# Kernel tuning notes

Measured on AMD Instinct MI355X. Metric: run time of the kernel, lower is better.

The kernel has to match this reference:

```python
import jax, jax.numpy as jnp
import numpy as np

INPUT_SIZE = 1024
HIDDEN_SIZE = 1024
BATCH = 32768
LEARNING_RATE = 0.01
# First call: time_stamps is empty -> temporal_weight = 1.0
TEMPORAL_WEIGHT = 1.0


def setup_inputs() -> dict:
    key = jax.random.key(0)
    kx, kw = jax.random.split(key)
    x = jax.random.normal(kx, (BATCH, INPUT_SIZE), dtype=jnp.float32)
    # nn.Parameter(torch.randn(input_size, hidden_size) * 0.1)
    W = jax.random.normal(kw, (INPUT_SIZE, HIDDEN_SIZE), dtype=jnp.float32) * 0.1
    return {"x": x, "W": W}


def reference(x, W):
    # Forward: hidden = tanh(x @ W)
    hidden = jnp.tanh(x @ W)  # [B, H]
    # Hebbian update: sum_b lr * outer(x_b, hidden_b) * w(t) / B == lr * w(t)/B * x^T @ hidden
    batch = x.shape[0]
    delta_w = (LEARNING_RATE * TEMPORAL_WEIGHT / batch) * (x.T @ hidden)  # [I, H]
    new_W = jnp.clip(W + delta_w, -1.0, 1.0)
    return hidden, new_W
```

## Files before the change

kernel.cpp:

```cpp
#include <hip/hip_runtime.h>
#include <hip/hip_fp8.h>
#include <cstdint>

#define BB 32768
#define II 1024
#define HH 1024
#define SPLIT 16
#define KCH (BB/SPLIT)
#define NT1 (II/64)
#define NT2 (KCH/64)

typedef _Float16 f16;
typedef _Float16 f16x4 __attribute__((ext_vector_type(4)));
typedef _Float16 f16x8 __attribute__((ext_vector_type(8)));
typedef float f32x4 __attribute__((ext_vector_type(4)));

typedef const __attribute__((address_space(1))) void gvoid_t;
typedef __attribute__((address_space(3))) void lvoid_t;

__device__ __forceinline__ void gload16(const void* g, void* l){
    __builtin_amdgcn_global_load_lds((gvoid_t*)g, (lvoid_t*)l, 16, 0, 0);
}

__device__ __forceinline__ float tanh_fast(float s){
    float a = fabsf(s);
    float e = __expf(-2.0f * a);
    float t = __fdividef(1.0f - e, 1.0f + e);
    return s < 0.0f ? -t : t;
}

__device__ __forceinline__ unsigned char f2fp8(float v){
    __hip_fp8_e4m3 q(v);
    return (unsigned char)q.__x;
}

__global__ __launch_bounds__(256) void k_prep2(const float* __restrict__ x,
                                               f16* __restrict__ xf,
                                               unsigned char* __restrict__ xt8,
                                               const float* __restrict__ W,
                                               f16* __restrict__ wt){
    __shared__ float lt[64*67];
    const int t = threadIdx.x;
    const int bx = (int)blockIdx.x;
    const bool isX = (bx < 512);
    const float* in = isX ? x : W;
    const int C = isX ? II : HH, R = isX ? BB : II;
    const int r0 = (isX ? bx : bx-512)*64;
    const int c0 = blockIdx.y*64;
    #pragma unroll
    for (int p=0; p<4; ++p){
        int r = p*16 + (t>>4);
        int c = (t&15)*4;
        f32x4 v = __builtin_nontemporal_load((const f32x4*)&in[(size_t)(r0+r)*C + c0 + c]);
        if (isX){
            f16x4 hv = {(f16)v[0],(f16)v[1],(f16)v[2],(f16)v[3]};
            *(f16x4*)&xf[(size_t)(r0+r)*C + c0 + c] = hv;
        }
        lt[r*67 + c+0] = v[0];
        lt[r*67 + c+1] = v[1];
        lt[r*67 + c+2] = v[2];
        lt[r*67 + c+3] = v[3];
    }
    __syncthreads();
    const int c = t>>2, rb = (t&3)*16;
    if (isX){
        union { unsigned char cb[16]; f32x4 v4; } u;
        #pragma unroll
        for (int e=0; e<16; ++e) u.cb[e] = f2fp8(lt[(rb+e)*67 + c]);
        *(f32x4*)&xt8[(size_t)(c0+c)*R + r0 + rb] = u.v4;
    } else {
        f16x8 a, b;
        #pragma unroll
        for (int e=0; e<8; ++e) a[e] = (f16)lt[(rb+e)*67 + c];
        #pragma unroll
        for (int e=0; e<8; ++e) b[e] = (f16)lt[(rb+8+e)*67 + c];
        f16* o = &wt[(size_t)(c0+c)*R + r0 + rb];
        *(f16x8*)o = a;
        *(f16x8*)(o+8) = b;
    }
}

__device__ __forceinline__ void stage_half(const f16* __restrict__ panel, int ld,
                                           int row0, int kcol0, char* lds_half,
                                           int wid, int lane){
    #pragma unroll
    for (int r=0;r<2;++r){
        int o = r*8192 + wid*1024 + lane*16;
        int rr = o>>7;
        int c0 = (o&127) ^ ((rr&7)<<4);
        gload16(panel + (size_t)(row0 + rr)*ld + kcol0 + (c0>>1), lds_half + r*8192 + wid*1024);
    }
}

#define RD_A(BUFA, mh) { \
    _Pragma("unroll") for (int m_=0;m_<4;++m_){ \
        af[m_][0] = *(const f16x8*)((BUFA) + rowA + (mh)*8192 + m_*2048 + ksw0); \
        af[m_][1] = *(const f16x8*)((BUFA) + rowA + (mh)*8192 + m_*2048 + ksw1); }}

#define RD_B(BUFB, nh) { \
    _Pragma("unroll") for (int n_=0;n_<2;++n_){ \
        bf[(nh)*2+n_][0] = *(const f16x8*)((BUFB) + rowB + (nh)*4096 + n_*2048 + ksw0); \
        bf[(nh)*2+n_][1] = *(const f16x8*)((BUFB) + rowB + (nh)*4096 + n_*2048 + ksw1); }}

#define MFMA_Q(mh,nh) { \
    __builtin_amdgcn_s_setprio(1); \
    _Pragma("unroll") for (int m_=0;m_<4;++m_){ \
      _Pragma("unroll") for (int n_=0;n_<2;++n_){ \
        _Pragma("unroll") for (int ks_=0;ks_<2;++ks_){ \
          acc[(mh)*4+m_][(nh)*2+n_] = __builtin_amdgcn_mfma_f32_16x16x32_f16( \
              af[m_][ks_], bf[(nh)*2+n_][ks_], acc[(mh)*4+m_][(nh)*2+n_], 0,0,0); }}} \
    __builtin_amdgcn_s_setprio(0); }

#define PH_SYNC1 { __builtin_amdgcn_s_barrier(); \
    asm volatile("s_waitcnt lgkmcnt(0)" ::: "memory"); \
    __builtin_amdgcn_sched_barrier(0); }
#define PH_SYNC2 { __builtin_amdgcn_s_barrier(); }
#define LGKM8 { asm volatile("s_waitcnt lgkmcnt(8)" ::: "memory"); }

__device__ __forceinline__ void kloop8_f16(const f16* __restrict__ Ap, int lda, int arow0,
                                           const f16* __restrict__ Bp, int ldb, int brow0,
                                           int kbase, int nt, char* sm,
                                           f32x4 (&acc)[8][4])
{
    const int t = threadIdx.x, lane = t & 63, wid = t >> 6;
    const int wr = wid >> 2, wc = wid & 3;
    const int fr = lane & 15, kg = lane >> 4;
    const int mask = nt - 1;
    char* const A0 = sm;
    char* const B0 = sm + 32768;
    char* const A1 = sm + 65536;
    char* const B1 = sm + 98304;
    const int rowA = wr*16384 + fr*128;
    const int rowB = (wc>>1)*16384 + (wc&1)*8192 + fr*128;
    const int ksw0 = ((kg    ) ^ (fr & 7)) << 4;
    const int ksw1 = ((kg + 4) ^ (fr & 7)) << 4;

    f16x8 af[4][2], bf[4][2];

    stage_half(Ap, lda, arow0 +   0, kbase +  0, A0,         wid, lane);
    stage_half(Ap, lda, arow0 + 128, kbase +  0, A0 + 16384, wid, lane);
    stage_half(Bp, ldb, brow0 +   0, kbase +  0, B0,         wid, lane);
    stage_half(Bp, ldb, brow0 + 128, kbase +  0, B0 + 16384, wid, lane);
    stage_half(Bp, ldb, brow0 +   0, kbase + 64, B1,         wid, lane);
    stage_half(Ap, lda, arow0 +   0, kbase + 64, A1,         wid, lane);
    asm volatile("s_waitcnt vmcnt(4)" ::: "memory");
    __builtin_amdgcn_s_barrier();

    const int ni = nt >> 1;
    for (int it = 0; it < ni; ++it){
        const int k1 = (2*it + 1) * 64;
        const int k2 = ((2*it + 2) & mask) * 64;
        const int k3 = ((2*it + 3) & mask) * 64;
        RD_A(A0, 0); RD_B(B0, 0);
        stage_half(Ap, lda, arow0 + 128, kbase + k1, A1 + 16384, wid, lane);
        LGKM8; PH_SYNC1; MFMA_Q(0,0); PH_SYNC2;
        RD_B(B0, 1);
        stage_half(Bp, ldb, brow0 + 128, kbase + k1, B1 + 16384, wid, lane);
        PH_SYNC1; MFMA_Q(0,1); PH_SYNC2;
        RD_A(A0, 1);
        stage_half(Bp, ldb, brow0 +   0, kbase + k2, B0, wid, lane);
        PH_SYNC1; MFMA_Q(1,0); PH_SYNC2;
        stage_half(Ap, lda, arow0 +   0, kbase + k2, A0, wid, lane);
        PH_SYNC1; MFMA_Q(1,1);
        asm volatile("s_waitcnt vmcnt(4)" ::: "memory");
        __builtin_amdgcn_s_barrier();
        RD_A(A1, 0); RD_B(B1, 0);
        stage_half(Ap, lda, arow0 + 128, kbase + k2, A0 + 16384, wid, lane);
        LGKM8; PH_SYNC1; MFMA_Q(0,0); PH_SYNC2;
        RD_B(B1, 1);
        stage_half(Bp, ldb, brow0 + 128, kbase + k2, B0 + 16384, wid, lane);
        PH_SYNC1; MFMA_Q(0,1); PH_SYNC2;
        RD_A(A1, 1);
        stage_half(Bp, ldb, brow0 +   0, kbase + k3, B1, wid, lane);
        PH_SYNC1; MFMA_Q(1,0); PH_SYNC2;
        stage_half(Ap, lda, arow0 +   0, kbase + k3, A1, wid, lane);
        PH_SYNC1; MFMA_Q(1,1);
        asm volatile("s_waitcnt vmcnt(4)" ::: "memory");
        __builtin_amdgcn_s_barrier();
    }
    asm volatile("s_waitcnt vmcnt(0)" ::: "memory");
    __builtin_amdgcn_s_barrier();
}

__global__ __launch_bounds__(512,2) void k_gemm1(const f16* __restrict__ xf,
                                                 const f16* __restrict__ wt,
                                                 float* __restrict__ hidden,
                                                 unsigned char* __restrict__ ht8){
    __shared__ char sm[131072];
    const int bid = (int)blockIdx.x;
    const int swz = (bid & 7)*64 + (bid >> 3);
    const int btile = swz >> 2, htile = swz & 3;
    f32x4 acc[8][4] = {};
    kloop8_f16(xf, II, btile*256, wt, II, htile*256, 0, NT1, sm, acc);

    const int t = threadIdx.x, lane = t & 63, wid = t >> 6;
    const int wr = wid >> 2, wc = wid & 3;
    const int fr = lane & 15, kg = lane >> 4;
    const int b_base = btile*256 + wr*128 + kg*4;
    const int h_base = htile*256 + wc*64 + fr;
    #pragma unroll
    for (int mf=0; mf<8; ++mf){
        const int b = b_base + mf*16;
        #pragma unroll
        for (int nf=0; nf<4; ++nf){
            const int h = h_base + nf*16;
            float t0 = tanh_fast(acc[mf][nf][0]);
            float t1 = tanh_fast(acc[mf][nf][1]);
            float t2 = tanh_fast(acc[mf][nf][2]);
            float t3 = tanh_fast(acc[mf][nf][3]);
            union { unsigned char cb[4]; unsigned int u; } p;
            p.cb[0] = f2fp8(t0); p.cb[1] = f2fp8(t1);
            p.cb[2] = f2fp8(t2); p.cb[3] = f2fp8(t3);
            *(unsigned int*)&ht8[(((size_t)(h>>4)*(BB>>4) + (b>>4))<<8) + ((h&15)<<4) + (b&15)] = p.u;
            hidden[(size_t)(b+0)*HH + h] = t0;
            hidden[(size_t)(b+1)*HH + h] = t1;
            hidden[(size_t)(b+2)*HH + h] = t2;
            hidden[(size_t)(b+3)*HH + h] = t3;
        }
    }
}

template<bool MT>
__device__ __forceinline__ void stage_half8(const unsigned char* __restrict__ panel, int ld,
                                            int row0, int kcol0, char* lds_half,
                                            int wid, int lane){
    int o  = wid*1024 + lane*16;
    int rr = o>>6;
    int c  = (o&63) ^ ((rr&6)<<3);
    if constexpr (!MT){
        gload16(panel + (size_t)(row0+rr)*ld + kcol0 + c, lds_half + wid*1024);
    } else {
        int h = row0 + rr;
        int babs = kcol0 + c;
        gload16(panel + (((size_t)(h>>4)*(BB>>4) + (babs>>4))<<8) + ((h&15)<<4) + (babs&15),
                lds_half + wid*1024);
    }
}

#define RD_A8(BUFA, mh) { \
    _Pragma("unroll") for (int m_=0;m_<4;++m_){ \
        afl[m_][0] = *(const long*)((BUFA) + rowA8 + (mh)*4096 + m_*1024 + k80); \
        afl[m_][1] = *(const long*)((BUFA) + rowA8 + (mh)*4096 + m_*1024 + k81); }}

#define RD_B8(BUFB, nh) { \
    _Pragma("unroll") for (int n_=0;n_<2;++n_){ \
        bfl[(nh)*2+n_][0] = *(const long*)((BUFB) + rowB8 + (nh)*2048 + n_*1024 + k80); \
        bfl[(nh)*2+n_][1] = *(const long*)((BUFB) + rowB8 + (nh)*2048 + n_*1024 + k81); }}

#define MFMA_Q8(mh,nh) { \
    __builtin_amdgcn_s_setprio(1); \
    _Pragma("unroll") for (int m_=0;m_<4;++m_){ \
      _Pragma("unroll") for (int n_=0;n_<2;++n_){ \
        _Pragma("unroll") for (int ks_=0;ks_<2;++ks_){ \
          acc[(mh)*4+m_][(nh)*2+n_] = __builtin_amdgcn_mfma_f32_16x16x32_fp8_fp8( \
              afl[m_][ks_], bfl[(nh)*2+n_][ks_], acc[(mh)*4+m_][(nh)*2+n_], 0,0,0); }}} \
    __builtin_amdgcn_s_setprio(0); }

__global__ __launch_bounds__(512,2) void k_gemm2(const unsigned char* __restrict__ xt8,
                                                 const unsigned char* __restrict__ ht8,
                                                 f16* __restrict__ part){
    __shared__ char sm[65536];
    const int bid = (int)blockIdx.x;
    const int swz = (bid & 7)*32 + (bid >> 3);
    const int split = swz >> 4, tile = swz & 15;
    const int itile = tile & 3, htile = tile >> 2;
    const int arow0 = itile*256, brow0 = htile*256, kbase = split*KCH;

    const int t = threadIdx.x, lane = t & 63, wid = t >> 6;
    const int wr = wid >> 2, wc = wid & 3;
    const int fr = lane & 15, kg = lane >> 4;
    const int mask = NT2 - 1;
    char* const A0 = sm;
    char* const B0 = sm + 16384;
    char* const A1 = sm + 32768;
    char* const B1 = sm + 49152;
    const int rowA8 = wr*8192 + fr*64;
    const int rowB8 = (wc>>1)*8192 + (wc&1)*4096 + fr*64;
    const int s6  = fr & 6;
    const int k80 = ((kg    ) ^ s6) << 3;
    const int k81 = ((kg + 4) ^ s6) << 3;

    f32x4 acc[8][4] = {};
    long afl[4][2], bfl[4][2];

    stage_half8<false>(xt8, BB, arow0 +   0, kbase +  0, A0,        wid, lane);
    stage_half8<false>(xt8, BB, arow0 + 128, kbase +  0, A0 + 8192, wid, lane);
    stage_half8<true >(ht8, BB, brow0 +   0, kbase +  0, B0,        wid, lane);
    stage_half8<true >(ht8, BB, brow0 + 128, kbase +  0, B0 + 8192, wid, lane);
    stage_half8<true >(ht8, BB, brow0 +   0, kbase + 64, B1,        wid, lane);
    stage_half8<false>(xt8, BB, arow0 +   0, kbase + 64, A1,        wid, lane);
    asm volatile("s_waitcnt vmcnt(2)" ::: "memory");
    __builtin_amdgcn_s_barrier();

    const int ni = NT2 >> 1;
    for (int it = 0; it < ni; ++it){
        const int k1 = (2*it + 1) * 64;
        const int k2 = ((2*it + 2) & mask) * 64;
        const int k3 = ((2*it + 3) & mask) * 64;
        RD_A8(A0, 0); RD_B8(B0, 0);
        stage_half8<false>(xt8, BB, arow0 + 128, kbase + k1, A1 + 8192, wid, lane);
        PH_SYNC1; MFMA_Q8(0,0); PH_SYNC2;
        RD_B8(B0, 1);
        stage_half8<true>(ht8, BB, brow0 + 128, kbase + k1, B1 + 8192, wid, lane);
        PH_SYNC1; MFMA_Q8(0,1); PH_SYNC2;
        RD_A8(A0, 1);
        stage_half8<true>(ht8, BB, brow0 +   0, kbase + k2, B0, wid, lane);
        PH_SYNC1; MFMA_Q8(1,0); PH_SYNC2;
        stage_half8<false>(xt8, BB, arow0 +   0, kbase + k2, A0, wid, lane);
        PH_SYNC1; MFMA_Q8(1,1);
        asm volatile("s_waitcnt vmcnt(2)" ::: "memory");
        __builtin_amdgcn_s_barrier();
        RD_A8(A1, 0); RD_B8(B1, 0);
        stage_half8<false>(xt8, BB, arow0 + 128, kbase + k2, A0 + 8192, wid, lane);
        PH_SYNC1; MFMA_Q8(0,0); PH_SYNC2;
        RD_B8(B1, 1);
        stage_half8<true>(ht8, BB, brow0 + 128, kbase + k2, B0 + 8192, wid, lane);
        PH_SYNC1; MFMA_Q8(0,1); PH_SYNC2;
        RD_A8(A1, 1);
        stage_half8<true>(ht8, BB, brow0 +   0, kbase + k3, B1, wid, lane);
        PH_SYNC1; MFMA_Q8(1,0); PH_SYNC2;
        stage_half8<false>(xt8, BB, arow0 +   0, kbase + k3, A1, wid, lane);
        PH_SYNC1; MFMA_Q8(1,1);
        asm volatile("s_waitcnt vmcnt(2)" ::: "memory");
        __builtin_amdgcn_s_barrier();
    }
    asm volatile("s_waitcnt vmcnt(0)" ::: "memory");
    __builtin_amdgcn_s_barrier();

    const size_t pb = (size_t)split*II*HH;
    #pragma unroll
    for (int mf=0; mf<8; ++mf){
        const int i0 = itile*256 + wr*128 + mf*16 + kg*4;
        #pragma unroll
        for (int nf=0; nf<4; ++nf){
            const int h = htile*256 + wc*64 + nf*16 + fr;
            f16x4 pv = {(f16)acc[mf][nf][0],(f16)acc[mf][nf][1],
                        (f16)acc[mf][nf][2],(f16)acc[mf][nf][3]};
            *(f16x4*)&part[pb + (((size_t)(i0>>4)*(HH>>4) + (h>>4))<<8) + ((h&15)<<4) + (i0&15)] = pv;
        }
    }
}

__global__ __launch_bounds__(256) void k_final(const f16* __restrict__ part,
                                               const float* __restrict__ W,
                                               float* __restrict__ outW){
    const int T = (int)blockIdx.x*256 + threadIdx.x;
    const int mt = T >> 5;
    const int hl = (T & 31) >> 1;
    const int ihalf = T & 1;
    const int i0 = (mt >> 6)*16 + ihalf*8;
    const int h  = (mt & 63)*16 + hl;
    const size_t po = ((size_t)mt << 8) + (hl << 4) + ihalf*8;
    float s[8] = {};
    #pragma unroll
    for (int sp=0; sp<SPLIT; ++sp){
        f16x8 p = __builtin_nontemporal_load((const f16x8*)&part[(size_t)sp*1048576 + po]);
        #pragma unroll
        for (int e=0;e<8;++e) s[e] += (float)p[e];
    }
    const float SCALE = 3.0517578125e-07f;
    #pragma unroll
    for (int e=0;e<8;++e){
        const size_t o = (size_t)(i0+e)*HH + h;
        float r = fminf(1.f, fmaxf(-1.f, fmaf(SCALE, s[e], W[o])));
        __builtin_nontemporal_store(r, &outW[o]);
    }
}

extern "C" void kernel_launch(void* const* d_in, const int* in_sizes, int n_in,
                              void* d_out, int out_size, void* d_ws, size_t ws_size,
                              hipStream_t stream){
    (void)in_sizes; (void)n_in; (void)out_size; (void)ws_size;
    const float* x = (const float*)d_in[0];
    const float* W = (const float*)d_in[1];
    float* hidden = (float*)d_out;
    float* outW   = hidden + (size_t)BB*HH;
    char* ws = (char*)d_ws;
    f16*           xf   = (f16*)(ws);
    unsigned char* xt8  = (unsigned char*)(ws + 67108864ull);
    unsigned char* ht8  = (unsigned char*)(ws + 100663296ull);
    f16*           wt   = (f16*)(ws + 134217728ull);
    f16*           part = (f16*)(ws);

    k_prep2<<<dim3(528, 16), 256, 0, stream>>>(x, xf, xt8, W, wt);
    k_gemm1<<<dim3((BB/256)*(HH/256)), 512, 0, stream>>>(xf, wt, hidden, ht8);
    k_gemm2<<<dim3(16*SPLIT), 512, 0, stream>>>(xt8, ht8, part);
    k_final<<<dim3((II*HH)/(256*8)), 256, 0, stream>>>(part, W, outW);
}
```

Before: 195.2 us.

## Peel last K iteration of gemm1 and interleave tanh epilogue with final MFMAs

```diff
diff --git a/kernel.cpp b/kernel.cpp
--- a/kernel.cpp
+++ b/kernel.cpp
@@ -116,16 +116,40 @@
     __builtin_amdgcn_sched_barrier(0); }
 #define PH_SYNC2 { __builtin_amdgcn_s_barrier(); }
 #define LGKM8 { asm volatile("s_waitcnt lgkmcnt(8)" ::: "memory"); }
-
-__device__ __forceinline__ void kloop8_f16(const f16* __restrict__ Ap, int lda, int arow0,
-                                           const f16* __restrict__ Bp, int ldb, int brow0,
-                                           int kbase, int nt, char* sm,
-                                           f32x4 (&acc)[8][4])
-{
+#define LGKM0SB { asm volatile("s_waitcnt lgkmcnt(0)" ::: "memory"); \
+    __builtin_amdgcn_sched_barrier(0); }
+
+#define EPI_Q(mh,nh) { \
+    _Pragma("unroll") for (int m_=0;m_<4;++m_){ \
+      const int b_ = b_base + ((mh)*4+m_)*16; \
+      _Pragma("unroll") for (int n_=0;n_<2;++n_){ \
+        const int h_ = h_base + ((nh)*2+n_)*16; \
+        float t0 = tanh_fast(acc[(mh)*4+m_][(nh)*2+n_][0]); \
+        float t1 = tanh_fast(acc[(mh)*4+m_][(nh)*2+n_][1]); \
+        float t2 = tanh_fast(acc[(mh)*4+m_][(nh)*2+n_][2]); \
+        float t3 = tanh_fast(acc[(mh)*4+m_][(nh)*2+n_][3]); \
+        union { unsigned char cb[4]; unsigned int u; } p_; \
+        p_.cb[0]=f2fp8(t0); p_.cb[1]=f2fp8(t1); p_.cb[2]=f2fp8(t2); p_.cb[3]=f2fp8(t3); \
+        *(unsigned int*)&ht8[(((size_t)(h_>>4)*(BB>>4) + (b_>>4))<<8) + ((h_&15)<<4) + (b_&15)] = p_.u; \
+        hidden[(size_t)(b_+0)*HH + h_] = t0; \
+        hidden[(size_t)(b_+1)*HH + h_] = t1; \
+        hidden[(size_t)(b_+2)*HH + h_] = t2; \
+        hidden[(size_t)(b_+3)*HH + h_] = t3; \
+    }}}
+
+__global__ __launch_bounds__(512,2) void k_gemm1(const f16* __restrict__ xf,
+                                                 const f16* __restrict__ wt,
+                                                 float* __restrict__ hidden,
+                                                 unsigned char* __restrict__ ht8){
+    __shared__ char sm[131072];
+    const int bid = (int)blockIdx.x;
+    const int swz = (bid & 7)*64 + (bid >> 3);
+    const int btile = swz >> 2, htile = swz & 3;
+    const int arow0 = btile*256, brow0 = htile*256;
+
     const int t = threadIdx.x, lane = t & 63, wid = t >> 6;
     const int wr = wid >> 2, wc = wid & 3;
     const int fr = lane & 15, kg = lane >> 4;
-    const int mask = nt - 1;
     char* const A0 = sm;
     char* const B0 = sm + 32768;
     char* const A1 = sm + 65536;
@@ -134,89 +158,74 @@
     const int rowB = (wc>>1)*16384 + (wc&1)*8192 + fr*128;
     const int ksw0 = ((kg    ) ^ (fr & 7)) << 4;
     const int ksw1 = ((kg + 4) ^ (fr & 7)) << 4;
-
+    const int b_base = btile*256 + wr*128 + kg*4;
+    const int h_base = htile*256 + wc*64 + fr;
+
+    f32x4 acc[8][4] = {};
     f16x8 af[4][2], bf[4][2];
 
-    stage_half(Ap, lda, arow0 +   0, kbase +  0, A0,         wid, lane);
-    stage_half(Ap, lda, arow0 + 128, kbase +  0, A0 + 16384, wid, lane);
-    stage_half(Bp, ldb, brow0 +   0, kbase +  0, B0,         wid, lane);
-    stage_half(Bp, ldb, brow0 + 128, kbase +  0, B0 + 16384, wid, lane);
-    stage_half(Bp, ldb, brow0 +   0, kbase + 64, B1,         wid, lane);
-    stage_half(Ap, lda, arow0 +   0, kbase + 64, A1,         wid, lane);
+    stage_half(xf, II, arow0 +   0,  0, A0,         wid, lane);
+    stage_half(xf, II, arow0 + 128,  0, A0 + 16384, wid, lane);
+    stage_half(wt, II, brow0 +   0,  0, B0,         wid, lane);
+    stage_half(wt, II, brow0 + 128,  0, B0 + 16384, wid, lane);
+    stage_half(wt, II, brow0 +   0, 64, B1,         wid, lane);
+    stage_half(xf, II, arow0 +   0, 64, A1,         wid, lane);
     asm volatile("s_waitcnt vmcnt(4)" ::: "memory");
     __builtin_amdgcn_s_barrier();
 
-    const int ni = nt >> 1;
-    for (int it = 0; it < ni; ++it){
+    const int ni = NT1 >> 1;
+    for (int it = 0; it < ni-1; ++it){
         const int k1 = (2*it + 1) * 64;
-        const int k2 = ((2*it + 2) & mask) * 64;
-        const int k3 = ((2*it + 3) & mask) * 64;
+        const int k2 = (2*it + 2) * 64;
+        const int k3 = (2*it + 3) * 64;
         RD_A(A0, 0); RD_B(B0, 0);
-        stage_half(Ap, lda, arow0 + 128, kbase + k1, A1 + 16384, wid, lane);
+        stage_half(xf, II, arow0 + 128, k1, A1 + 16384, wid, lane);
         LGKM8; PH_SYNC1; MFMA_Q(0,0); PH_SYNC2;
         RD_B(B0, 1);
-        stage_half(Bp, ldb, brow0 + 128, kbase + k1, B1 + 16384, wid, lane);
+        stage_half(wt, II, brow0 + 128, k1, B1 + 16384, wid, lane);
         PH_SYNC1; MFMA_Q(0,1); PH_SYNC2;
         RD_A(A0, 1);
-        stage_half(Bp, ldb, brow0 +   0, kbase + k2, B0, wid, lane);
+        stage_half(wt, II, brow0 +   0, k2, B0, wid, lane);
         PH_SYNC1; MFMA_Q(1,0); PH_SYNC2;
-        stage_half(Ap, lda, arow0 +   0, kbase + k2, A0, wid, lane);
+        stage_half(xf, II, arow0 +   0, k2, A0, wid, lane);
         PH_SYNC1; MFMA_Q(1,1);
         asm volatile("s_waitcnt vmcnt(4)" ::: "memory");
         __builtin_amdgcn_s_barrier();
         RD_A(A1, 0); RD_B(B1, 0);
-        stage_half(Ap, lda, arow0 + 128, kbase + k2, A0 + 16384, wid, lane);
+        stage_half(xf, II, arow0 + 128, k2, A0 + 16384, wid, lane);
         LGKM8; PH_SYNC1; MFMA_Q(0,0); PH_SYNC2;
         RD_B(B1, 1);
-        stage_half(Bp, ldb, brow0 + 128, kbase + k2, B0 + 16384, wid, lane);
+        stage_half(wt, II, brow0 + 128, k2, B0 + 16384, wid, lane);
         PH_SYNC1; MFMA_Q(0,1); PH_SYNC2;
         RD_A(A1, 1);
-        stage_half(Bp, ldb, brow0 +   0, kbase + k3, B1, wid, lane);
+        stage_half(wt, II, brow0 +   0, k3, B1, wid, lane);
         PH_SYNC1; MFMA_Q(1,0); PH_SYNC2;
-        stage_half(Ap, lda, arow0 +   0, kbase + k3, A1, wid, lane);
+        stage_half(xf, II, arow0 +   0, k3, A1, wid, lane);
         PH_SYNC1; MFMA_Q(1,1);
         asm volatile("s_waitcnt vmcnt(4)" ::: "memory");
         __builtin_amdgcn_s_barrier();
     }
-    asm volatile("s_waitcnt vmcnt(0)" ::: "memory");
-    __builtin_amdgcn_s_barrier();
-}
-
-__global__ __launch_bounds__(512,2) void k_gemm1(const f16* __restrict__ xf,
-                                                 const f16* __restrict__ wt,
-                                                 float* __restrict__ hidden,
-                                                 unsigned char* __restrict__ ht8){
-    __shared__ char sm[131072];
-    const int bid = (int)blockIdx.x;
-    const int swz = (bid & 7)*64 + (bid >> 3);
-    const int btile = swz >> 2, htile = swz & 3;
-    f32x4 acc[8][4] = {};
-    kloop8_f16(xf, II, btile*256, wt, II, htile*256, 0, NT1, sm, acc);
-
-    const int t = threadIdx.x, lane = t & 63, wid = t >> 6;
-    const int wr = wid >> 2, wc = wid & 3;
-    const int fr = lane & 15, kg = lane >> 4;
-    const int b_base = btile*256 + wr*128 + kg*4;
-    const int h_base = htile*256 + wc*64 + fr;
-    #pragma unroll
-    for (int mf=0; mf<8; ++mf){
-        const int b = b_base + mf*16;
-        #pragma unroll
-        for (int nf=0; nf<4; ++nf){
-            const int h = h_base + nf*16;
-            float t0 = tanh_fast(acc[mf][nf][0]);
-            float t1 = tanh_fast(acc[mf][nf][1]);
-            float t2 = tanh_fast(acc[mf][nf][2]);
-            float t3 = tanh_fast(acc[mf][nf][3]);
-            union { unsigned char cb[4]; unsigned int u; } p;
-            p.cb[0] = f2fp8(t0); p.cb[1] = f2fp8(t1);
-            p.cb[2] = f2fp8(t2); p.cb[3] = f2fp8(t3);
-            *(unsigned int*)&ht8[(((size_t)(h>>4)*(BB>>4) + (b>>4))<<8) + ((h&15)<<4) + (b&15)] = p.u;
-            hidden[(size_t)(b+0)*HH + h] = t0;
-            hidden[(size_t)(b+1)*HH + h] = t1;
-            hidden[(size_t)(b+2)*HH + h] = t2;
-            hidden[(size_t)(b+3)*HH + h] = t3;
-        }
+
+    {
+        const int kL = (NT1-1)*64;
+        RD_A(A0, 0); RD_B(B0, 0);
+        stage_half(xf, II, arow0 + 128, kL, A1 + 16384, wid, lane);
+        LGKM0SB; MFMA_Q(0,0);
+        RD_B(B0, 1);
+        stage_half(wt, II, brow0 + 128, kL, B1 + 16384, wid, lane);
+        LGKM0SB; MFMA_Q(0,1);
+        RD_A(A0, 1);
+        LGKM0SB; MFMA_Q(1,0);
+        MFMA_Q(1,1);
+        asm volatile("s_waitcnt vmcnt(0)" ::: "memory");
+        __builtin_amdgcn_s_barrier();
+        RD_A(A1, 0); RD_B(B1, 0);
+        LGKM0SB; MFMA_Q(0,0); EPI_Q(0,0);
+        RD_B(B1, 1);
+        LGKM0SB; MFMA_Q(0,1); EPI_Q(0,1);
+        RD_A(A1, 1);
+        LGKM0SB; MFMA_Q(1,0); EPI_Q(1,0);
+        MFMA_Q(1,1); EPI_Q(1,1);
     }
 }
 
```

Result: no change. 192.7 us (median of 2 runs) (-1.2%).

## Rewrite forward GEMM with 256x128 tiles and triple-buffered K=32 pipeline

Applied to the files above, without the earlier changes.

```diff
diff --git a/kernel.cpp b/kernel.cpp
--- a/kernel.cpp
+++ b/kernel.cpp
@@ -7,7 +7,7 @@
 #define HH 1024
 #define SPLIT 16
 #define KCH (BB/SPLIT)
-#define NT1 (II/64)
+#define NT1_32 (II/32)
 #define NT2 (KCH/64)
 
 typedef _Float16 f16;
@@ -80,137 +80,81 @@
     }
 }
 
-__device__ __forceinline__ void stage_half(const f16* __restrict__ panel, int ld,
-                                           int row0, int kcol0, char* lds_half,
-                                           int wid, int lane){
-    #pragma unroll
-    for (int r=0;r<2;++r){
-        int o = r*8192 + wid*1024 + lane*16;
-        int rr = o>>7;
-        int c0 = (o&127) ^ ((rr&7)<<4);
-        gload16(panel + (size_t)(row0 + rr)*ld + kcol0 + (c0>>1), lds_half + r*8192 + wid*1024);
-    }
-}
-
-#define RD_A(BUFA, mh) { \
-    _Pragma("unroll") for (int m_=0;m_<4;++m_){ \
-        af[m_][0] = *(const f16x8*)((BUFA) + rowA + (mh)*8192 + m_*2048 + ksw0); \
-        af[m_][1] = *(const f16x8*)((BUFA) + rowA + (mh)*8192 + m_*2048 + ksw1); }}
-
-#define RD_B(BUFB, nh) { \
-    _Pragma("unroll") for (int n_=0;n_<2;++n_){ \
-        bf[(nh)*2+n_][0] = *(const f16x8*)((BUFB) + rowB + (nh)*4096 + n_*2048 + ksw0); \
-        bf[(nh)*2+n_][1] = *(const f16x8*)((BUFB) + rowB + (nh)*4096 + n_*2048 + ksw1); }}
-
-#define MFMA_Q(mh,nh) { \
-    __builtin_amdgcn_s_setprio(1); \
-    _Pragma("unroll") for (int m_=0;m_<4;++m_){ \
-      _Pragma("unroll") for (int n_=0;n_<2;++n_){ \
-        _Pragma("unroll") for (int ks_=0;ks_<2;++ks_){ \
-          acc[(mh)*4+m_][(nh)*2+n_] = __builtin_amdgcn_mfma_f32_16x16x32_f16( \
-              af[m_][ks_], bf[(nh)*2+n_][ks_], acc[(mh)*4+m_][(nh)*2+n_], 0,0,0); }}} \
-    __builtin_amdgcn_s_setprio(0); }
-
-#define PH_SYNC1 { __builtin_amdgcn_s_barrier(); \
-    asm volatile("s_waitcnt lgkmcnt(0)" ::: "memory"); \
-    __builtin_amdgcn_sched_barrier(0); }
-#define PH_SYNC2 { __builtin_amdgcn_s_barrier(); }
-#define LGKM8 { asm volatile("s_waitcnt lgkmcnt(8)" ::: "memory"); }
-
-__device__ __forceinline__ void kloop8_f16(const f16* __restrict__ Ap, int lda, int arow0,
-                                           const f16* __restrict__ Bp, int ldb, int brow0,
-                                           int kbase, int nt, char* sm,
-                                           f32x4 (&acc)[8][4])
-{
+__global__ __launch_bounds__(512,4) void k_gemm1(const f16* __restrict__ xf,
+                                                 const f16* __restrict__ wt,
+                                                 float* __restrict__ hidden,
+                                                 unsigned char* __restrict__ ht8){
+    __shared__ char sm[73728];
+    const int bid = (int)blockIdx.x;
+    const int swz = (bid & 7)*128 + (bid >> 3);
+    const int btile = swz >> 3, htile = swz & 7;
+    const int arow0 = btile*256, brow0 = htile*128;
     const int t = threadIdx.x, lane = t & 63, wid = t >> 6;
     const int wr = wid >> 2, wc = wid & 3;
     const int fr = lane & 15, kg = lane >> 4;
-    const int mask = nt - 1;
-    char* const A0 = sm;
-    char* const B0 = sm + 32768;
-    char* const A1 = sm + 65536;
-    char* const B1 = sm + 98304;
-    const int rowA = wr*16384 + fr*128;
-    const int rowB = (wc>>1)*16384 + (wc&1)*8192 + fr*128;
-    const int ksw0 = ((kg    ) ^ (fr & 7)) << 4;
-    const int ksw1 = ((kg + 4) ^ (fr & 7)) << 4;
-
-    f16x8 af[4][2], bf[4][2];
-
-    stage_half(Ap, lda, arow0 +   0, kbase +  0, A0,         wid, lane);
-    stage_half(Ap, lda, arow0 + 128, kbase +  0, A0 + 16384, wid, lane);
-    stage_half(Bp, ldb, brow0 +   0, kbase +  0, B0,         wid, lane);
-    stage_half(Bp, ldb, brow0 + 128, kbase +  0, B0 + 16384, wid, lane);
-    stage_half(Bp, ldb, brow0 +   0, kbase + 64, B1,         wid, lane);
-    stage_half(Ap, lda, arow0 +   0, kbase + 64, A1,         wid, lane);
-    asm volatile("s_waitcnt vmcnt(4)" ::: "memory");
-    __builtin_amdgcn_s_barrier();
-
-    const int ni = nt >> 1;
-    for (int it = 0; it < ni; ++it){
-        const int k1 = (2*it + 1) * 64;
-        const int k2 = ((2*it + 2) & mask) * 64;
-        const int k3 = ((2*it + 3) & mask) * 64;
-        RD_A(A0, 0); RD_B(B0, 0);
-        stage_half(Ap, lda, arow0 + 128, kbase + k1, A1 + 16384, wid, lane);
-        LGKM8; PH_SYNC1; MFMA_Q(0,0); PH_SYNC2;
-        RD_B(B0, 1);
-        stage_half(Bp, ldb, brow0 + 128, kbase + k1, B1 + 16384, wid, lane);
-        PH_SYNC1; MFMA_Q(0,1); PH_SYNC2;
-        RD_A(A0, 1);
-        stage_half(Bp, ldb, brow0 +   0, kbase + k2, B0, wid, lane);
-        PH_SYNC1; MFMA_Q(1,0); PH_SYNC2;
-        stage_half(Ap, lda, arow0 +   0, kbase + k2, A0, wid, lane);
-        PH_SYNC1; MFMA_Q(1,1);
-        asm volatile("s_waitcnt vmcnt(4)" ::: "memory");
+    const int rowA = (wr*128 + fr)*64;
+    const int rowB = (wc*32 + fr)*64;
+    const int ksw  = ((kg ^ ((fr>>1)&3)) << 4);
+
+    f32x4 acc[8][2] = {};
+    f16x8 af[8], bf[2];
+
+    const int oA0 = wid*1024 + lane*16;
+    #define STAGE_A(KC, BUF) { \
+        _Pragma("unroll") for (int s_=0;s_<2;++s_){ \
+            int o_ = s_*8192 + oA0; \
+            int rr_ = o_>>6; \
+            int c_ = (o_&63) ^ (((rr_>>1)&3)<<4); \
+            gload16(xf + (size_t)(arow0+rr_)*II + (KC) + (c_>>1), (BUF) + s_*8192 + wid*1024); }}
+    #define STAGE_B(KC, BUF) { \
+        int o_ = oA0; \
+        int rr_ = o_>>6; \
+        int c_ = (o_&63) ^ (((rr_>>1)&3)<<4); \
+        gload16(wt + (size_t)(brow0+rr_)*II + (KC) + (c_>>1), (BUF) + wid*1024); }
+
+    STAGE_A(0,  sm);          STAGE_B(0,  sm + 16384);
+    STAGE_A(32, sm + 24576);  STAGE_B(32, sm + 24576 + 16384);
+
+    for (int tt = 0; tt < NT1_32; ++tt){
+        if (tt < NT1_32-1){ asm volatile("s_waitcnt vmcnt(3)" ::: "memory"); }
+        else              { asm volatile("s_waitcnt vmcnt(0)" ::: "memory"); }
         __builtin_amdgcn_s_barrier();
-        RD_A(A1, 0); RD_B(B1, 0);
-        stage_half(Ap, lda, arow0 + 128, kbase + k2, A0 + 16384, wid, lane);
-        LGKM8; PH_SYNC1; MFMA_Q(0,0); PH_SYNC2;
-        RD_B(B1, 1);
-        stage_half(Bp, ldb, brow0 + 128, kbase + k2, B0 + 16384, wid, lane);
-        PH_SYNC1; MFMA_Q(0,1); PH_SYNC2;
-        RD_A(A1, 1);
-        stage_half(Bp, ldb, brow0 +   0, kbase + k3, B1, wid, lane);
-        PH_SYNC1; MFMA_Q(1,0); PH_SYNC2;
-        stage_half(Ap, lda, arow0 +   0, kbase + k3, A1, wid, lane);
-        PH_SYNC1; MFMA_Q(1,1);
-        asm volatile("s_waitcnt vmcnt(4)" ::: "memory");
-        __builtin_amdgcn_s_barrier();
-    }
-    asm volatile("s_waitcnt vmcnt(0)" ::: "memory");
-    __builtin_amdgcn_s_barrier();
-}
-
-__global__ __launch_bounds__(512,2) void k_gemm1(const f16* __restrict__ xf,
-                                                 const f16* __restrict__ wt,
-                                                 float* __restrict__ hidden,
-                                                 unsigned char* __restrict__ ht8){
-    __shared__ char sm[131072];
-    const int bid = (int)blockIdx.x;
-    const int swz = (bid & 7)*64 + (bid >> 3);
-    const int btile = swz >> 2, htile = swz & 3;
-    f32x4 acc[8][4] = {};
-    kloop8_f16(xf, II, btile*256, wt, II, htile*256, 0, NT1, sm, acc);
-
-    const int t = threadIdx.x, lane = t & 63, wid = t >> 6;
-    const int wr = wid >> 2, wc = wid & 3;
-    const int fr = lane & 15, kg = lane >> 4;
+        char* const Ac = sm + (tt%3)*24576;
+        char* const Bc = Ac + 16384;
+        #pragma unroll
+        for (int m=0;m<8;++m) af[m] = *(const f16x8*)(Ac + rowA + m*1024 + ksw);
+        #pragma unroll
+        for (int n=0;n<2;++n) bf[n] = *(const f16x8*)(Bc + rowB + n*1024 + ksw);
+        asm volatile("s_waitcnt lgkmcnt(0)" ::: "memory");
+        __builtin_amdgcn_sched_barrier(0);
+        if (tt + 2 < NT1_32){
+            char* const Nn = sm + ((tt+2)%3)*24576;
+            STAGE_A((tt+2)*32, Nn);
+            STAGE_B((tt+2)*32, Nn + 16384);
+        }
+        __builtin_amdgcn_s_setprio(1);
+        #pragma unroll
+        for (int m=0;m<8;++m)
+            #pragma unroll
+            for (int n=0;n<2;++n)
+                acc[m][n] = __builtin_amdgcn_mfma_f32_16x16x32_f16(af[m], bf[n], acc[m][n], 0, 0, 0);
+        __builtin_amdgcn_s_setprio(0);
+    }
+
     const int b_base = btile*256 + wr*128 + kg*4;
-    const int h_base = htile*256 + wc*64 + fr;
+    const int h_base = htile*128 + wc*32 + fr;
     #pragma unroll
     for (int mf=0; mf<8; ++mf){
         const int b = b_base + mf*16;
         #pragma unroll
-        for (int nf=0; nf<4; ++nf){
+        for (int nf=0; nf<2; ++nf){
             const int h = h_base + nf*16;
             float t0 = tanh_fast(acc[mf][nf][0]);
             float t1 = tanh_fast(acc[mf][nf][1]);
             float t2 = tanh_fast(acc[mf][nf][2]);
             float t3 = tanh_fast(acc[mf][nf][3]);
             union { unsigned char cb[4]; unsigned int u; } p;
-            p.cb[0] = f2fp8(t0); p.cb[1] = f2fp8(t1);
-            p.cb[2] = f2fp8(t2); p.cb[3] = f2fp8(t3);
+            p.cb[0]=f2fp8(t0); p.cb[1]=f2fp8(t1); p.cb[2]=f2fp8(t2); p.cb[3]=f2fp8(t3);
             *(unsigned int*)&ht8[(((size_t)(h>>4)*(BB>>4) + (b>>4))<<8) + ((h&15)<<4) + (b&15)] = p.u;
             hidden[(size_t)(b+0)*HH + h] = t0;
             hidden[(size_t)(b+1)*HH + h] = t1;
@@ -219,6 +163,11 @@
         }
     }
 }
+
+#define PH_SYNC1 { __builtin_amdgcn_s_barrier(); \
+    asm volatile("s_waitcnt lgkmcnt(0)" ::: "memory"); \
+    __builtin_amdgcn_sched_barrier(0); }
+#define PH_SYNC2 { __builtin_amdgcn_s_barrier(); }
 
 template<bool MT>
 __device__ __forceinline__ void stage_half8(const unsigned char* __restrict__ panel, int ld,
@@ -383,7 +332,7 @@
     f16*           part = (f16*)(ws);
 
     k_prep2<<<dim3(528, 16), 256, 0, stream>>>(x, xf, xt8, W, wt);
-    k_gemm1<<<dim3((BB/256)*(HH/256)), 512, 0, stream>>>(xf, wt, hidden, ht8);
+    k_gemm1<<<dim3((BB/256)*(HH/128)), 512, 0, stream>>>(xf, wt, hidden, ht8);
     k_gemm2<<<dim3(16*SPLIT), 512, 0, stream>>>(xt8, ht8, part);
     k_final<<<dim3((II*HH)/(256*8)), 256, 0, stream>>>(part, W, outW);
 }
```

After: 203.0 us. 4.0% more time.
